# Performance work log

Measured on AMD Instinct MI355X. Metric: run time of the kernel, lower is better.

## Reference

```python
import jax, jax.numpy as jnp
import numpy as np

BATCH = 256
B_TYPES = 32   # input capsule types
C_TYPES = 10   # output capsule types
H, W = 8, 8    # input spatial extent == kernel (output is 1x1)
POSE = 16      # capsule pose length (shape (16,1))
NUM_ITER = 3
EPS = 1e-8


def setup_inputs() -> dict:
    key = jax.random.key(0)
    k1, k2, k3 = jax.random.split(key, 3)
    input_caps_poses = jax.random.normal(k1, (BATCH, B_TYPES, H, W, POSE, 1), jnp.float32)
    input_caps_activations = jax.random.uniform(k2, (BATCH, B_TYPES, H, W), jnp.float32)
    # nn.init.normal_(std=0.1) on [B, kh, kw, C, os0, is0]
    weight = 0.1 * jax.random.normal(k3, (B_TYPES, H, W, C_TYPES, POSE, POSE), jnp.float32)
    # routing_bias initialized to 0.1: [C, oh, ow, os0, os1]
    routing_bias = jnp.full((C_TYPES, 1, 1, POSE, 1), 0.1, jnp.float32)
    return {
        "input_caps_poses": input_caps_poses,
        "input_caps_activations": input_caps_activations,
        "weight": weight,
        "routing_bias": routing_bias,
    }


def _squash(s):
    # Hinton squash: ||s||^2/(1+||s||^2) * s/||s||, norm over pose dims
    n2 = jnp.sum(s * s, axis=(-2, -1), keepdims=True)
    return (n2 / (1.0 + n2)) * s * jax.lax.rsqrt(n2 + EPS)


def reference(input_caps_poses, input_caps_activations, weight, routing_bias):
    b = input_caps_poses.shape[0]
    # votes[b,c,B,h,w,o,p] = sum_i W[B,h,w,c,o,i] * pose[b,B,h,w,i,p]
    votes = jnp.einsum('Bhwcoi,bBhwip->bcBhwop', weight, input_caps_poses)
    logits = jnp.zeros((b, C_TYPES, B_TYPES, H, W), votes.dtype)
    bias = routing_bias.reshape(1, C_TYPES, POSE, 1)
    v = None
    for it in range(NUM_ITER):
        # coupling coefficients: softmax over output capsule types
        c = jax.nn.softmax(logits, axis=1)                      # [b,C,B,h,w]
        # weighted sum of votes over all input capsules (B,h,w)
        s = jnp.einsum('bcBhw,bcBhwop->bcop', c, votes) + bias  # [b,C,16,1]
        v = _squash(s)
        if it < NUM_ITER - 1:
            # agreement: dot(vote, output pose)
            logits = logits + jnp.einsum('bcBhwop,bcop->bcBhw', votes, v)
    output_caps_poses = v[:, :, None, None, :, :]               # [b,C,1,1,16,1]
    output_caps_activations = jnp.sqrt(
        jnp.sum(v * v, axis=(-2, -1)) + EPS)[:, :, None, None]  # [b,C,1,1]
    return output_caps_poses, output_caps_activations
```

## Files before the change

### kernel.cpp

```cpp
#include <hip/hip_runtime.h>
#include <hip/hip_fp16.h>
#include <math.h>


typedef _Float16 f16;
typedef _Float16 f16x2 __attribute__((ext_vector_type(2)));
typedef _Float16 f16x4 __attribute__((ext_vector_type(4)));
typedef __fp16   h16x2 __attribute__((ext_vector_type(2)));
typedef float f32x4 __attribute__((ext_vector_type(4)));

__device__ __forceinline__ f16x2 pk(float a, float b) {
    h16x2 t = __builtin_amdgcn_cvt_pkrtz(a, b);
    return __builtin_bit_cast(f16x2, t);
}

#if __has_builtin(__builtin_amdgcn_fdot2)
__device__ __forceinline__ float FDOT2(f16x2 a, f16x2 b, float c) {
    return __builtin_amdgcn_fdot2(__builtin_bit_cast(h16x2, a),
                                  __builtin_bit_cast(h16x2, b), c, false);
}
#else
__device__ __forceinline__ float FDOT2(f16x2 a, f16x2 b, float c) {
    return c + (float)a[0] * (float)b[0] + (float)a[1] * (float)b[1];
}
#endif

constexpr int WS_ROW = 28;
constexpr int XS_ROW = 76;

__device__ __forceinline__ float xorsum4(float v) {
    v += __shfl_xor(v, 16, 64);
    v += __shfl_xor(v, 32, 64);
    return v;
}

__device__ __forceinline__ f16x2 xorsum4h(f16x2 v) {
    union { f16x2 h; int i; } u;
    union { int i; f16x2 h; } w;
    u.h = v; w.i = __shfl_xor(u.i, 16, 64); v = v + w.h;
    u.h = v; w.i = __shfl_xor(u.i, 32, 64); v = v + w.h;
    return v;
}

__device__ __forceinline__ f16x4 cvt4(float4 w) {
    f16x2 a = pk(w.x, w.y);
    f16x2 b = pk(w.z, w.w);
    f16x4 r; r[0] = a[0]; r[1] = a[1]; r[2] = b[0]; r[3] = b[1];
    return r;
}

template<int PASS>
__global__ __launch_bounds__(256, 2)
void pass_k(const float* __restrict__ poses, const float* __restrict__ weight,
            const float* __restrict__ bias,
            const float* __restrict__ sp0, const float* __restrict__ sp1,
            float* __restrict__ s_dst)
{
    __shared__ f16 Ws[640 * WS_ROW];
    __shared__ f16 xs[64 * XS_ROW];

    const int tid  = threadIdx.x;
    const int blk  = blockIdx.x;
    const int ngrp = blk >> 2;
    const int b0   = (blk & 3) * 64;
    const int wave = tid >> 6;
    const int lane = tid & 63;
    const int q    = lane >> 4;
    const int lo   = lane & 15;
    const int wtb  = wave * 16;
    const int bg   = b0 + wtb;

    float4 wreg[10];
    float4 xreg[4];
    const int b_loc = tid >> 2, part = tid & 3;

    auto load_w = [&](int l) {
        const float* wp = weight + (size_t)(ngrp * 4 + l) * 10240;
        #pragma unroll
        for (int k = 0; k < 10; ++k) wreg[k] = ((const float4*)wp)[tid + k * 256];
    };
    auto load_x = [&](int l) {
        const float* xp = poses + (size_t)(b0 + b_loc) * 32768
                          + (size_t)(ngrp * 16 + l * 4 + part) * 16;
        #pragma unroll
        for (int j = 0; j < 4; ++j) xreg[j] = ((const float4*)xp)[j];
    };
    auto store_iter = [&]() {
        #pragma unroll
        for (int k = 0; k < 10; ++k) {
            const int f = tid + k * 256;
            *(f16x4*)&Ws[(f >> 2) * WS_ROW + (f & 3) * 4] = cvt4(wreg[k]);
        }
        f16* lp = xs + b_loc * XS_ROW + part * 16;
        #pragma unroll
        for (int j = 0; j < 4; ++j) *(f16x4*)&lp[j * 4] = cvt4(xreg[j]);
    };

    load_w(0);

    f16x2 vsp[10][2];
    if (PASS >= 1) {
        const int rowb = (bg + lo) * 10;
        #pragma unroll
        for (int c = 0; c < 10; ++c) {
            float4 bb = *(const float4*)(bias + c * 16 + q * 4);
            float4 sa = *(const float4*)(sp0 + (size_t)(rowb + c) * 16 + q * 4);
            float t0 = sa.x + bb.x, t1 = sa.y + bb.y, t2 = sa.z + bb.z, t3 = sa.w + bb.w;
            float n2 = xorsum4(t0*t0 + t1*t1 + t2*t2 + t3*t3);
            float sc = n2 / (1.f + n2) * rsqrtf(n2 + 1e-8f);
            float v0 = sc*t0, v1 = sc*t1, v2 = sc*t2, v3 = sc*t3;
            if (PASS == 2) {
                float4 sb = *(const float4*)(sp1 + (size_t)(rowb + c) * 16 + q * 4);
                float u0 = sb.x + bb.x, u1 = sb.y + bb.y, u2 = sb.z + bb.z, u3 = sb.w + bb.w;
                float m2 = xorsum4(u0*u0 + u1*u1 + u2*u2 + u3*u3);
                float sc2 = m2 / (1.f + m2) * rsqrtf(m2 + 1e-8f);
                v0 += sc2*u0; v1 += sc2*u1; v2 += sc2*u2; v3 += sc2*u3;
            }
            vsp[c][0] = pk(v0, v1);
            vsp[c][1] = pk(v2, v3);
        }
    }

    load_x(0);

    f32x4 acc[10];
    #pragma unroll
    for (int c = 0; c < 10; ++c) acc[c] = (f32x4){0.f, 0.f, 0.f, 0.f};

    for (int l = 0; l < 4; ++l) {
        __syncthreads();
        store_iter();
        if (l + 1 < 4) { load_w(l + 1); load_x(l + 1); }
        __syncthreads();

        #pragma unroll
        for (int n = 0; n < 4; ++n) {
            f16x4 bx = *(const f16x4*)&xs[(wtb + lo) * XS_ROW + n * 16 + q * 4];
            f16x2 Vh[10][2];
            #pragma unroll
            for (int c = 0; c < 10; ++c) {
                f16x4 aw = *(const f16x4*)&Ws[((n * 10 + c) * 16 + lo) * WS_ROW + q * 4];
                f32x4 V = __builtin_amdgcn_mfma_f32_16x16x16f16(
                    aw, bx, (f32x4){0.f, 0.f, 0.f, 0.f}, 0, 0, 0);
                Vh[c][0] = pk(V[0], V[1]);
                Vh[c][1] = pk(V[2], V[3]);
            }

            float cfv[10];
            if (PASS >= 1) {
                float lg[10];
                #pragma unroll
                for (int cp = 0; cp < 5; ++cp) {
                    const int c0 = cp * 2, c1 = cp * 2 + 1;
                    float p0 = FDOT2(Vh[c0][0], vsp[c0][0], 0.f);
                    p0 = FDOT2(Vh[c0][1], vsp[c0][1], p0);
                    float p1 = FDOT2(Vh[c1][0], vsp[c1][0], 0.f);
                    p1 = FDOT2(Vh[c1][1], vsp[c1][1], p1);
                    f16x2 pr = xorsum4h(pk(p0, p1));
                    lg[c0] = (float)pr[0];
                    lg[c1] = (float)pr[1];
                }
                float m = lg[0];
                #pragma unroll
                for (int c = 1; c < 10; ++c) m = fmaxf(m, lg[c]);
                float sum = 0.f;
                #pragma unroll
                for (int c = 0; c < 10; ++c) { lg[c] = __expf(lg[c] - m); sum += lg[c]; }
                const float inv = 1.f / sum;
                #pragma unroll
                for (int c = 0; c < 10; ++c) cfv[c] = lg[c] * inv;
            }

            #pragma unroll
            for (int c = 0; c < 10; ++c) {
                const float w = (PASS == 0) ? 1.f : cfv[c];
                acc[c][0] = fmaf(w, (float)Vh[c][0][0], acc[c][0]);
                acc[c][1] = fmaf(w, (float)Vh[c][0][1], acc[c][1]);
                acc[c][2] = fmaf(w, (float)Vh[c][1][0], acc[c][2]);
                acc[c][3] = fmaf(w, (float)Vh[c][1][1], acc[c][3]);
            }
        }
    }

    __syncthreads();
    float* tr = (float*)Ws + wave * 320;
    const float fs = (PASS == 0) ? 0.1f : 1.f;
    #pragma unroll
    for (int c = 0; c < 10; ++c) {
        *(float4*)&tr[lo * 20 + q * 4] = (float4){acc[c][0], acc[c][1], acc[c][2], acc[c][3]};
        float r0 = tr[(q * 4 + 0) * 20 + lo];
        float r1 = tr[(q * 4 + 1) * 20 + lo];
        float r2 = tr[(q * 4 + 2) * 20 + lo];
        float r3 = tr[(q * 4 + 3) * 20 + lo];
        float* sp = s_dst + ((size_t)(bg + q * 4) * 10 + c) * 16 + lo;
        unsafeAtomicAdd(sp + 0 * 160, fs * r0);
        unsafeAtomicAdd(sp + 1 * 160, fs * r1);
        unsafeAtomicAdd(sp + 2 * 160, fs * r2);
        unsafeAtomicAdd(sp + 3 * 160, fs * r3);
    }
}

__global__ __launch_bounds__(256)
void epi_k(const float* __restrict__ s2, const float* __restrict__ bias,
           float* __restrict__ out)
{
    const int t = blockIdx.x * 256 + threadIdx.x;
    if (t >= 2560) return;
    const int c = t % 10;
    const float* sp = s2 + (size_t)t * 16;
    const float* bp = bias + c * 16;
    float sv[16];
    float n2 = 0.f;
    #pragma unroll
    for (int o = 0; o < 16; ++o) { float v = sp[o] + bp[o]; sv[o] = v; n2 += v * v; }
    const float scale = n2 / (1.f + n2) * rsqrtf(n2 + 1e-8f);
    float a2 = 0.f;
    #pragma unroll
    for (int o = 0; o < 16; ++o) {
        float v = scale * sv[o];
        out[(size_t)t * 16 + o] = v;
        a2 += v * v;
    }
    out[40960 + t] = sqrtf(a2 + 1e-8f);
}

extern "C" void kernel_launch(void* const* d_in, const int* in_sizes, int n_in,
                              void* d_out, int out_size, void* d_ws, size_t ws_size,
                              hipStream_t stream)
{
    const float* poses  = (const float*)d_in[0];
    const float* weight = (const float*)d_in[2];
    const float* bias   = (const float*)d_in[3];
    float* out = (float*)d_out;
    float* s0 = (float*)d_ws;
    float* s1 = s0 + 40960;
    float* s2 = s1 + 40960;

    (void)hipMemsetAsync(d_ws, 0, 3 * 40960 * sizeof(float), stream);

    pass_k<0><<<512, 256, 0, stream>>>(poses, weight, bias, nullptr, nullptr, s0);
    pass_k<1><<<512, 256, 0, stream>>>(poses, weight, bias, s0, nullptr, s1);
    pass_k<2><<<512, 256, 0, stream>>>(poses, weight, bias, s0, s1, s2);
    epi_k<<<10, 256, 0, stream>>>(s2, bias, out);
}
```

Before: 201.5 us.

## Double-buffer LDS tiles with XOR swizzle and one barrier per iteration

Weight and pose tiles are now kept in two LDS buffers, so the next tile is converted and stored while the current one is being consumed. This cuts the two barriers per iteration to one. The padded weight row stride is replaced by an XOR-swizzled 16-element row, which avoids bank conflicts without padding. LDS use per block rises to about 60KB, which can limit occupancy, and the global loads are issued later relative to their use.

```diff
diff --git a/kernel.cpp b/kernel.cpp
--- a/kernel.cpp
+++ b/kernel.cpp
@@ -25,7 +25,6 @@
 }
 #endif
 
-constexpr int WS_ROW = 28;
 constexpr int XS_ROW = 76;
 
 __device__ __forceinline__ float xorsum4(float v) {
@@ -56,8 +55,8 @@
             const float* __restrict__ sp0, const float* __restrict__ sp1,
             float* __restrict__ s_dst)
 {
-    __shared__ f16 Ws[640 * WS_ROW];
-    __shared__ f16 xs[64 * XS_ROW];
+    __shared__ f16 Ws[2][640 * 16];
+    __shared__ f16 xs[2][64 * XS_ROW];
 
     const int tid  = threadIdx.x;
     const int blk  = blockIdx.x;
@@ -70,9 +69,14 @@
     const int wtb  = wave * 16;
     const int bg   = b0 + wtb;
 
+    const int sr  = ((lo >> 1) ^ (lo >> 3)) & 3;
+    const int xqE = ((q ^ sr) & 3) * 4;
+    const int xqO = ((q ^ sr ^ 2) & 3) * 4;
+
     float4 wreg[10];
     float4 xreg[4];
     const int b_loc = tid >> 2, part = tid & 3;
+    const int wcol = (((tid & 3) ^ ((tid >> 3) ^ (tid >> 5))) & 3) * 4;
 
     auto load_w = [&](int l) {
         const float* wp = weight + (size_t)(ngrp * 4 + l) * 10240;
@@ -85,13 +89,13 @@
         #pragma unroll
         for (int j = 0; j < 4; ++j) xreg[j] = ((const float4*)xp)[j];
     };
-    auto store_iter = [&]() {
+    auto store_iter = [&](int buf) {
         #pragma unroll
         for (int k = 0; k < 10; ++k) {
             const int f = tid + k * 256;
-            *(f16x4*)&Ws[(f >> 2) * WS_ROW + (f & 3) * 4] = cvt4(wreg[k]);
-        }
-        f16* lp = xs + b_loc * XS_ROW + part * 16;
+            *(f16x4*)&Ws[buf][(f >> 2) * 16 + wcol] = cvt4(wreg[k]);
+        }
+        f16* lp = xs[buf] + b_loc * XS_ROW + part * 16;
         #pragma unroll
         for (int j = 0; j < 4; ++j) *(f16x4*)&lp[j * 4] = cvt4(xreg[j]);
     };
@@ -121,25 +125,27 @@
         }
     }
 
+    f32x4 acc[10];
+    #pragma unroll
+    for (int c = 0; c < 10; ++c) acc[c] = (f32x4){0.f, 0.f, 0.f, 0.f};
+
     load_x(0);
-
-    f32x4 acc[10];
-    #pragma unroll
-    for (int c = 0; c < 10; ++c) acc[c] = (f32x4){0.f, 0.f, 0.f, 0.f};
-
+    store_iter(0);
+    load_w(1);
+    __syncthreads();
+
+    #pragma unroll 1
     for (int l = 0; l < 4; ++l) {
-        __syncthreads();
-        store_iter();
-        if (l + 1 < 4) { load_w(l + 1); load_x(l + 1); }
-        __syncthreads();
+        const int buf = l & 1;
 
         #pragma unroll
         for (int n = 0; n < 4; ++n) {
-            f16x4 bx = *(const f16x4*)&xs[(wtb + lo) * XS_ROW + n * 16 + q * 4];
+            f16x4 bx = *(const f16x4*)&xs[buf][(wtb + lo) * XS_ROW + n * 16 + q * 4];
             f16x2 Vh[10][2];
             #pragma unroll
             for (int c = 0; c < 10; ++c) {
-                f16x4 aw = *(const f16x4*)&Ws[((n * 10 + c) * 16 + lo) * WS_ROW + q * 4];
+                f16x4 aw = *(const f16x4*)&Ws[buf][((n * 10 + c) * 16 + lo) * 16
+                                                   + ((c & 1) ? xqO : xqE)];
                 f32x4 V = __builtin_amdgcn_mfma_f32_16x16x16f16(
                     aw, bx, (f32x4){0.f, 0.f, 0.f, 0.f}, 0, 0, 0);
                 Vh[c][0] = pk(V[0], V[1]);
@@ -180,10 +186,16 @@
                 acc[c][3] = fmaf(w, (float)Vh[c][1][1], acc[c][3]);
             }
         }
-    }
-
-    __syncthreads();
-    float* tr = (float*)Ws + wave * 320;
+
+        if (l < 3) {
+            load_x(l + 1);
+            store_iter((l + 1) & 1);
+            if (l < 2) load_w(l + 2);
+            __syncthreads();
+        }
+    }
+
+    float* tr = (float*)&Ws[0][0] + wave * 320;
     const float fs = (PASS == 0) ? 0.1f : 1.f;
     #pragma unroll
     for (int c = 0; c < 10; ++c) {
```

Result: slower. 212.5 us (+5.5%).

## Fuse three routing passes and epilogue into one cooperative kernel with grid sync

Applied to the files above, without the earlier changes.

Replaces the three per-pass kernel launches and the epilogue launch with a single cooperative kernel that loops over passes, separated by threadfence plus grid.sync, and then runs the squash epilogue in-kernel. The aim is to remove launch gaps and kernel boundaries between the dependent passes. It turns the pass index into a runtime value, which may cost registers or branch specialisation. It relies on 512 blocks being co-resident (2 per CU via launch bounds), and falls back to separate launches if the cooperative launch fails.

```diff
diff --git a/kernel.cpp b/kernel.cpp
--- a/kernel.cpp
+++ b/kernel.cpp
@@ -1,6 +1,9 @@
 #include <hip/hip_runtime.h>
 #include <hip/hip_fp16.h>
+#include <hip/hip_cooperative_groups.h>
 #include <math.h>
+
+namespace cg = cooperative_groups;
 
 
 typedef _Float16 f16;
@@ -49,16 +52,15 @@
     return r;
 }
 
-template<int PASS>
-__global__ __launch_bounds__(256, 2)
-void pass_k(const float* __restrict__ poses, const float* __restrict__ weight,
-            const float* __restrict__ bias,
-            const float* __restrict__ sp0, const float* __restrict__ sp1,
-            float* __restrict__ s_dst)
-{
-    __shared__ f16 Ws[640 * WS_ROW];
-    __shared__ f16 xs[64 * XS_ROW];
-
+template<bool FUSED>
+__device__ __forceinline__ void pass_body(
+    int pass,
+    const float* __restrict__ poses, const float* __restrict__ weight,
+    const float* __restrict__ bias,
+    const float* __restrict__ sp0, const float* __restrict__ sp1,
+    float* __restrict__ s_dst,
+    f16* Ws, f16* xs)
+{
     const int tid  = threadIdx.x;
     const int blk  = blockIdx.x;
     const int ngrp = blk >> 2;
@@ -99,7 +101,7 @@
     load_w(0);
 
     f16x2 vsp[10][2];
-    if (PASS >= 1) {
+    if (pass >= 1) {
         const int rowb = (bg + lo) * 10;
         #pragma unroll
         for (int c = 0; c < 10; ++c) {
@@ -109,7 +111,7 @@
             float n2 = xorsum4(t0*t0 + t1*t1 + t2*t2 + t3*t3);
             float sc = n2 / (1.f + n2) * rsqrtf(n2 + 1e-8f);
             float v0 = sc*t0, v1 = sc*t1, v2 = sc*t2, v3 = sc*t3;
-            if (PASS == 2) {
+            if (pass == 2) {
                 float4 sb = *(const float4*)(sp1 + (size_t)(rowb + c) * 16 + q * 4);
                 float u0 = sb.x + bb.x, u1 = sb.y + bb.y, u2 = sb.z + bb.z, u3 = sb.w + bb.w;
                 float m2 = xorsum4(u0*u0 + u1*u1 + u2*u2 + u3*u3);
@@ -147,7 +149,7 @@
             }
 
             float cfv[10];
-            if (PASS >= 1) {
+            if (pass >= 1) {
                 float lg[10];
                 #pragma unroll
                 for (int cp = 0; cp < 5; ++cp) {
@@ -173,7 +175,7 @@
 
             #pragma unroll
             for (int c = 0; c < 10; ++c) {
-                const float w = (PASS == 0) ? 1.f : cfv[c];
+                const float w = (pass == 0) ? 1.f : cfv[c];
                 acc[c][0] = fmaf(w, (float)Vh[c][0][0], acc[c][0]);
                 acc[c][1] = fmaf(w, (float)Vh[c][0][1], acc[c][1]);
                 acc[c][2] = fmaf(w, (float)Vh[c][1][0], acc[c][2]);
@@ -184,7 +186,7 @@
 
     __syncthreads();
     float* tr = (float*)Ws + wave * 320;
-    const float fs = (PASS == 0) ? 0.1f : 1.f;
+    const float fs = (pass == 0) ? 0.1f : 1.f;
     #pragma unroll
     for (int c = 0; c < 10; ++c) {
         *(float4*)&tr[lo * 20 + q * 4] = (float4){acc[c][0], acc[c][1], acc[c][2], acc[c][3]};
@@ -198,6 +200,58 @@
         unsafeAtomicAdd(sp + 2 * 160, fs * r2);
         unsafeAtomicAdd(sp + 3 * 160, fs * r3);
     }
+}
+
+__global__ __launch_bounds__(256, 2)
+void fused_k(const float* __restrict__ poses, const float* __restrict__ weight,
+             const float* __restrict__ bias,
+             float* __restrict__ s0, float* __restrict__ s1,
+             float* __restrict__ s2, float* __restrict__ out)
+{
+    __shared__ f16 Ws[640 * WS_ROW];
+    __shared__ f16 xs[64 * XS_ROW];
+
+    cg::grid_group grid = cg::this_grid();
+
+    #pragma unroll 1
+    for (int pass = 0; pass < 3; ++pass) {
+        float* dst = (pass == 0) ? s0 : (pass == 1) ? s1 : s2;
+        pass_body<true>(pass, poses, weight, bias, s0, s1, dst, Ws, xs);
+        __threadfence();
+        grid.sync();
+    }
+
+    const int t = blockIdx.x * 256 + threadIdx.x;
+    if (t < 2560) {
+        const int c = t % 10;
+        const float* sp = s2 + (size_t)t * 16;
+        const float* bp = bias + c * 16;
+        float sv[16];
+        float n2 = 0.f;
+        #pragma unroll
+        for (int o = 0; o < 16; ++o) { float v = sp[o] + bp[o]; sv[o] = v; n2 += v * v; }
+        const float scale = n2 / (1.f + n2) * rsqrtf(n2 + 1e-8f);
+        float a2 = 0.f;
+        #pragma unroll
+        for (int o = 0; o < 16; ++o) {
+            float v = scale * sv[o];
+            out[(size_t)t * 16 + o] = v;
+            a2 += v * v;
+        }
+        out[40960 + t] = sqrtf(a2 + 1e-8f);
+    }
+}
+
+template<int PASS>
+__global__ __launch_bounds__(256, 2)
+void pass_k(const float* __restrict__ poses, const float* __restrict__ weight,
+            const float* __restrict__ bias,
+            const float* __restrict__ sp0, const float* __restrict__ sp1,
+            float* __restrict__ s_dst)
+{
+    __shared__ f16 Ws[640 * WS_ROW];
+    __shared__ f16 xs[64 * XS_ROW];
+    pass_body<false>(PASS, poses, weight, bias, sp0, sp1, s_dst, Ws, xs);
 }
 
 __global__ __launch_bounds__(256)
@@ -238,8 +292,15 @@
 
     (void)hipMemsetAsync(d_ws, 0, 3 * 40960 * sizeof(float), stream);
 
-    pass_k<0><<<512, 256, 0, stream>>>(poses, weight, bias, nullptr, nullptr, s0);
-    pass_k<1><<<512, 256, 0, stream>>>(poses, weight, bias, s0, nullptr, s1);
-    pass_k<2><<<512, 256, 0, stream>>>(poses, weight, bias, s0, s1, s2);
-    epi_k<<<10, 256, 0, stream>>>(s2, bias, out);
-}
+    void* args[] = {(void*)&poses, (void*)&weight, (void*)&bias,
+                    (void*)&s0, (void*)&s1, (void*)&s2, (void*)&out};
+    hipError_t err = hipLaunchCooperativeKernel((const void*)fused_k,
+                                                dim3(512), dim3(256),
+                                                args, 0, stream);
+    if (err != hipSuccess) {
+        pass_k<0><<<512, 256, 0, stream>>>(poses, weight, bias, nullptr, nullptr, s0);
+        pass_k<1><<<512, 256, 0, stream>>>(poses, weight, bias, s0, nullptr, s1);
+        pass_k<2><<<512, 256, 0, stream>>>(poses, weight, bias, s0, s1, s2);
+        epi_k<<<10, 256, 0, stream>>>(s2, bias, out);
+    }
+}
```

Result: slower. 670.9 us (+232.9%).
